# Kernel tuning notes

Measured on AMD Instinct MI355X. Metric: run time of the kernel, lower is better.

Reference implementation:

```python
import jax, jax.numpy as jnp
import numpy as np

EPS = 1e-12


def pairwise_sqdist(x, y):
    # x: (B, N, 3), y: (B, M, 3) -> (B, N, M) squared euclidean distances
    xx = jnp.sum(x * x, axis=-1)              # (B, N)
    yy = jnp.sum(y * y, axis=-1)              # (B, M)
    xy = jnp.einsum('bnd,bmd->bnm', x, y)     # (B, N, M)
    d = xx[:, :, None] + yy[None_ if False else yy[:, None, :].shape and 0 or ...] if False else xx[:, :, None] + yy[:, None, :] - 2.0 * xy
    return jnp.maximum(d, 0.0)


def chamfer_l1(x, y):
    # pytorch3d/PoinTr-style ChamferDistanceL1:
    # mean over points of sqrt(min squared dist), averaged over both directions
    d = pairwise_sqdist(x, y)                 # (B, N, M)
    d1 = jnp.min(d, axis=2)                   # (B, N) x -> nearest y
    d2 = jnp.min(d, axis=1)                   # (B, M) y -> nearest x
    d1 = jnp.sqrt(jnp.maximum(d1, EPS))
    d2 = jnp.sqrt(jnp.maximum(d2, EPS))
    return 0.5 * (jnp.mean(d1) + jnp.mean(d2))


def knn1_gather(x, y):
    # For each point in x (B,N,3), find nearest neighbor in y (B,M,3) (K=1)
    # and gather it -> (B, N, 3). Matches knn_points + knn_gather + squeeze.
    d = pairwise_sqdist(x, y)                 # (B, N, M)
    idx = jnp.argmin(d, axis=2)               # (B, N) int
    return jnp.take_along_axis(y, idx[:, :, None], axis=1)  # (B, N, 3)


def volume_with_wedge(p):
    # wedge-product volume over consecutive point triples:
    # V = sum_i (p_i x p_{i+1}) . p_{i+2} / 6  -> (B,)
    c = jnp.cross(p[:, :-2, :], p[:, 1:-1, :])  # (B, N-2, 3)
    return jnp.sum(jnp.einsum('bnd,bnd->bn', c, p[:, 2:, :]), axis=-1) / 6.0


def setup_inputs() -> dict:
    key = jax.random.key(0)
    k1, k2, k3 = jax.random.split(key, 3)
    B, Nc, Nf, M = 2, 512, 8192, 8192
    return {
        'source_coarse': jax.random.normal(k1, (B, Nc, 3), dtype=jnp.float32),
        'source_fine': jax.random.normal(k2, (B, Nf, 3), dtype=jnp.float32),
        'target_points': jax.random.normal(k3, (B, M, 3), dtype=jnp.float32),
    }


def reference(source_coarse, source_fine, target_points):
    lambda_rot = lambda_ref = lambda_align = lambda_geo = 1.0
    B = source_fine.shape[0]
    axis = jnp.broadcast_to(jnp.array([0.0, 0.0, 1.0], dtype=source_fine.dtype), (B, 3))
    plane_normal = jnp.broadcast_to(jnp.array([0.0, 1.0, 0.0], dtype=source_fine.dtype), (B, 3))

    # KNN (K=1) gather of nearest target point for each fine source point
    new_target = knn1_gather(source_fine, target_points)  # (B, Nf, 3)

    # alignment (Chamfer L1) losses
    loss_align_coarse = chamfer_l1(source_coarse, target_points)
    loss_align_fine = chamfer_l1(source_fine, target_points)

    # rotational symmetry loss
    in_proj = jnp.einsum('bij,bj->bi', source_fine, axis)      # (B, Nf)
    re_proj = jnp.einsum('bij,bj->bi', new_target, axis)
    loss_rot = jnp.mean((jnp.linalg.norm(in_proj, axis=-1) - jnp.linalg.norm(re_proj, axis=-1)) ** 2)

    # reflectional symmetry loss
    pn = plane_normal / jnp.linalg.norm(plane_normal, axis=-1, keepdims=True)
    in_dist = jnp.einsum('bij,bj->bi', source_fine, pn)
    re_dist = jnp.einsum('bij,bj->bi', new_target, pn)
    loss_ref = jnp.mean((in_dist - re_dist) ** 2)

    # geometric consistency (wedge-product volume) loss
    loss_geo = jnp.mean((volume_with_wedge(source_fine) - volume_with_wedge(new_target)) ** 2)

    total = (lambda_rot * loss_rot + lambda_ref * loss_ref
             + lambda_align * loss_align_coarse + lambda_align * loss_align_fine
             + lambda_geo * loss_geo)
    return total
```

## Files before the change

### kernel.cpp

```cpp
#include <hip/hip_runtime.h>
#include <stdint.h>
#include <float.h>

using u64 = unsigned long long;
typedef float v2f __attribute__((ext_vector_type(2)));

constexpr int B_ = 2;
constexpr int NC = 512;
constexpr int NF = 8192;
constexpr int MT = 8192;

constexpr int TPB = 256;
constexpr int CFF = 32;
constexpr int CCR = 128;
constexpr int CCC = 8;
constexpr int TAIL_BLOCKS = 196;

#define DEVINL __device__ __forceinline__

template<bool ARGMIN, int R2t, int NJ>
DEVINL void pairmin_phase(const float* __restrict__ P, const float* __restrict__ Q,
                          int nP, int nQ, int b, int row_base, int j0,
                          int chunk, int nRowsTot,
                          u64* __restrict__ outPack, unsigned* __restrict__ outVal)
{
#pragma clang fp contract(off)
    const int tid = threadIdx.x;

    v2f tx0[R2t], tx1[R2t], tx2[R2t], txx[R2t], dbest[R2t];
    int jb[2 * R2t];
    #pragma unroll
    for (int r = 0; r < R2t; ++r) {
        const int row0 = row_base + tid + (2 * r) * TPB;
        const int row1 = row_base + tid + (2 * r + 1) * TPB;
        const float* p0 = P + ((size_t)b * nP + row0) * 3;
        const float* p1 = P + ((size_t)b * nP + row1) * 3;
        float a0 = p0[0], a1 = p0[1], a2 = p0[2];
        float e0 = p1[0], e1 = p1[1], e2 = p1[2];
        tx0[r] = v2f{2.0f * a0, 2.0f * e0};
        tx1[r] = v2f{2.0f * a1, 2.0f * e1};
        tx2[r] = v2f{2.0f * a2, 2.0f * e2};
        txx[r] = v2f{(a0*a0 + a1*a1) + a2*a2, (e0*e0 + e1*e1) + e2*e2};
        dbest[r] = v2f{FLT_MAX, FLT_MAX};
        jb[2 * r] = 0; jb[2 * r + 1] = 0;
    }

    const float* qbase = Q + (size_t)b * nQ * 3;

    float q0r[8], q1r[8], q2r[8];
    #pragma unroll
    for (int u = 0; u < 8; ++u) {
        const float* qp = qbase + (size_t)(j0 + u) * 3;
        q0r[u] = qp[0]; q1r[u] = qp[1]; q2r[u] = qp[2];
    }

    for (int jj = 0; jj < NJ; jj += 8) {
        #pragma unroll
        for (int u = 0; u < 8; ++u) {
            const float q0 = q0r[u], q1 = q1r[u], q2 = q2r[u];
            int pj = jj + 8 + u;  pj = (pj < NJ) ? pj : (NJ - 1);
            const float* qp = qbase + (size_t)(j0 + pj) * 3;
            q0r[u] = qp[0]; q1r[u] = qp[1]; q2r[u] = qp[2];

            const float qq = (q0*q0 + q1*q1) + q2*q2;
            const int j = j0 + jj + u;
            #pragma unroll
            for (int r = 0; r < R2t; ++r) {
                v2f s = (tx0[r] * q0 + tx1[r] * q1) + tx2[r] * q2;
                v2f d = (txx[r] + qq) - s;
                if (ARGMIN) {
                    bool c0 = d.x < dbest[r].x;
                    bool c1 = d.y < dbest[r].y;
                    dbest[r].x = c0 ? d.x : dbest[r].x;
                    dbest[r].y = c1 ? d.y : dbest[r].y;
                    jb[2 * r]     = c0 ? j : jb[2 * r];
                    jb[2 * r + 1] = c1 ? j : jb[2 * r + 1];
                } else {
                    dbest[r] = __builtin_elementwise_min(dbest[r], d);
                }
            }
        }
    }

    const v2f vzero = {0.0f, 0.0f};
    const size_t o0 = (size_t)chunk * nRowsTot + (size_t)b * nP;
    #pragma unroll
    for (int r = 0; r < R2t; ++r) {
        v2f dcl = __builtin_elementwise_max(dbest[r], vzero);
        const int row0 = row_base + tid + (2 * r) * TPB;
        const int row1 = row_base + tid + (2 * r + 1) * TPB;
        if (ARGMIN) {
            outPack[o0 + row0] = ((u64)__float_as_uint(dcl.x) << 32) | (unsigned)jb[2 * r];
            outPack[o0 + row1] = ((u64)__float_as_uint(dcl.y) << 32) | (unsigned)jb[2 * r + 1];
        } else {
            outVal[o0 + row0] = __float_as_uint(dcl.x);
            outVal[o0 + row1] = __float_as_uint(dcl.y);
        }
    }
}

__global__ __launch_bounds__(TPB, 4) void pairmin_all(
    const float* __restrict__ coarse, const float* __restrict__ fine,
    const float* __restrict__ tgt,
    u64* __restrict__ pfr, unsigned* __restrict__ pfc,
    unsigned* __restrict__ pcr, unsigned* __restrict__ pcc,
    unsigned* __restrict__ counter)
{
    const int bx = blockIdx.x;
    if (bx == 0 && threadIdx.x == 0) *counter = 0;
    const int b   = bx >> 8;
    const int sub = bx & 255;
    const int g   = sub >> 5;
    const int c   = sub & 31;

    pairmin_phase<true, 2, 256>(fine, tgt, NF, MT, b, g * 1024, c * 256,
                                c, B_ * NF, pfr, nullptr);
    pairmin_phase<false, 2, 256>(tgt, fine, MT, NF, b, g * 1024, c * 256,
                                 c, B_ * MT, nullptr, pfc);
    if (sub < 128) {
        pairmin_phase<false, 1, 64>(coarse, tgt, NC, MT, b, 0, sub * 64,
                                    sub, B_ * NC, nullptr, pcr);
    } else {
        const int s2 = sub - 128;
        const int rg = s2 & 15;
        const int jc = s2 >> 4;
        pairmin_phase<false, 1, 64>(tgt, coarse, MT, NC, b, rg * 512, jc * 64,
                                    jc, B_ * MT, nullptr, pcc);
    }
}

__global__ __launch_bounds__(TPB) void tail_all(
    const float* __restrict__ fine, const float* __restrict__ tgt,
    const u64* __restrict__ pfr, const unsigned* __restrict__ pfc,
    const unsigned* __restrict__ pcr, const unsigned* __restrict__ pcc,
    double* __restrict__ bs, unsigned* __restrict__ counter,
    float* __restrict__ out)
{
    __shared__ float sp[TPB + 2][3], yp[TPB + 2][3];
    __shared__ double redw[4][9];
    __shared__ double lred[4][13];
    __shared__ int lastflag;
    const int bx = blockIdx.x, tid = threadIdx.x;
    const int wave = tid >> 6, lane = tid & 63;

    double v_s = 0, v_d2f = 0, v_d1c = 0, v_d2c = 0, v_yd2 = 0, v_zs = 0, v_zt = 0;
    double vs = 0, vt = 0;
    int role_b = 0;

    if (bx < 64) {
        const int base = bx * TPB;
        const int g = base + tid;
        const int b = base >> 13;  role_b = b;
        u64 best = pfr[g];
        #pragma unroll
        for (int cc = 1; cc < CFF; ++cc) {
            u64 p = pfr[(size_t)cc * (B_ * NF) + g];
            best = p < best ? p : best;
        }
        float d1 = __uint_as_float((unsigned)(best >> 32));
        int idx  = (int)(best & 0xffffffffULL);
        float s = sqrtf(fmaxf(d1, 1e-12f));
        const float* y  = tgt  + ((size_t)b * MT + idx) * 3;
        const float* sr = fine + (size_t)g * 3;
        float y0 = y[0],  y1 = y[1],  y2 = y[2];
        float s0 = sr[0], s1 = sr[1], s2 = sr[2];
        yp[tid][0] = y0; yp[tid][1] = y1; yp[tid][2] = y2;
        sp[tid][0] = s0; sp[tid][1] = s1; sp[tid][2] = s2;
        const int base_b = base & (NF - 1);
        if (tid < 2 && base_b + TPB + tid < NF) {
            int g2 = base + TPB + tid;
            u64 b2 = pfr[g2];
            #pragma unroll
            for (int cc = 1; cc < CFF; ++cc) {
                u64 p = pfr[(size_t)cc * (B_ * NF) + g2];
                b2 = p < b2 ? p : b2;
            }
            int i2 = (int)(b2 & 0xffffffffULL);
            const float* yh = tgt  + ((size_t)b * MT + i2) * 3;
            const float* sh = fine + (size_t)g2 * 3;
            #pragma unroll
            for (int k = 0; k < 3; ++k) { yp[TPB + tid][k] = yh[k]; sp[TPB + tid][k] = sh[k]; }
        }
        __syncthreads();
        v_s = s;
        float yd = s1 - y1;
        v_yd2 = (double)(yd * yd);
        v_zs  = (double)(s2 * s2);
        v_zt  = (double)(y2 * y2);
        int rb = base_b + tid;
        if (rb <= NF - 3) {
            {
                const float* a = sp[tid]; const float* c2 = sp[tid+1]; const float* e = sp[tid+2];
                float c0 = a[1]*c2[2] - a[2]*c2[1];
                float c1 = a[2]*c2[0] - a[0]*c2[2];
                float c2v = a[0]*c2[1] - a[1]*c2[0];
                vs = (double)(c0*e[0] + c1*e[1] + c2v*e[2]);
            }
            {
                const float* a = yp[tid]; const float* c2 = yp[tid+1]; const float* e = yp[tid+2];
                float c0 = a[1]*c2[2] - a[2]*c2[1];
                float c1 = a[2]*c2[0] - a[0]*c2[2];
                float c2v = a[0]*c2[1] - a[1]*c2[0];
                vt = (double)(c0*e[0] + c1*e[1] + c2v*e[2]);
            }
        }
    } else if (bx < 128) {
        const int g = (bx - 64) * TPB + tid;
        unsigned best = pfc[g];
        #pragma unroll
        for (int cc = 1; cc < CFF; ++cc) best = min(best, pfc[(size_t)cc * (B_ * MT) + g]);
        v_d2f = (double)sqrtf(fmaxf(__uint_as_float(best), 1e-12f));
    } else if (bx < 132) {
        const int g = (bx - 128) * TPB + tid;
        unsigned best = pcr[g];
        #pragma unroll 16
        for (int cc = 1; cc < CCR; ++cc) best = min(best, pcr[(size_t)cc * (B_ * NC) + g]);
        v_d1c = (double)sqrtf(fmaxf(__uint_as_float(best), 1e-12f));
    } else {
        const int g = (bx - 132) * TPB + tid;
        unsigned best = pcc[g];
        #pragma unroll
        for (int cc = 1; cc < CCC; ++cc) best = min(best, pcc[(size_t)cc * (B_ * MT) + g]);
        v_d2c = (double)sqrtf(fmaxf(__uint_as_float(best), 1e-12f));
    }

    double r9[9] = {v_s, v_d2f, v_d1c, v_d2c, v_yd2, v_zs, v_zt, vs, vt};
    for (int o = 32; o; o >>= 1) {
        #pragma unroll
        for (int k = 0; k < 9; ++k) r9[k] += __shfl_down(r9[k], o);
    }
    if (lane == 0) {
        #pragma unroll
        for (int k = 0; k < 9; ++k) redw[wave][k] = r9[k];
    }
    __syncthreads();
    if (tid == 0) {
        double t9[9];
        #pragma unroll
        for (int k = 0; k < 9; ++k)
            t9[k] = redw[0][k] + redw[1][k] + redw[2][k] + redw[3][k];
        double* o = bs + (size_t)bx * 16;
        #pragma unroll
        for (int k = 0; k < 16; ++k) o[k] = 0.0;
        o[0] = t9[0]; o[1] = t9[1]; o[2] = t9[2]; o[3] = t9[3]; o[4] = t9[4];
        o[5 + role_b]  = t9[5];
        o[7 + role_b]  = t9[6];
        o[9 + role_b]  = t9[7];
        o[11 + role_b] = t9[8];
        __threadfence();
        unsigned old = atomicAdd(counter, 1u);
        lastflag = (old == TAIL_BLOCKS - 1);
    }
    __syncthreads();
    if (!lastflag) return;

    __threadfence();
    double c13[13];
    if (tid < TAIL_BLOCKS) {
        const double* p = bs + (size_t)tid * 16;
        #pragma unroll
        for (int k = 0; k < 13; ++k) c13[k] = p[k];
    } else {
        #pragma unroll
        for (int k = 0; k < 13; ++k) c13[k] = 0.0;
    }
    for (int o = 32; o; o >>= 1) {
        #pragma unroll
        for (int k = 0; k < 13; ++k) c13[k] += __shfl_down(c13[k], o);
    }
    if (lane == 0) {
        #pragma unroll
        for (int k = 0; k < 13; ++k) lred[wave][k] = c13[k];
    }
    __syncthreads();
    if (tid == 0) {
        double S[13];
        #pragma unroll
        for (int k = 0; k < 13; ++k)
            S[k] = lred[0][k] + lred[1][k] + lred[2][k] + lred[3][k];
        double m_d1f = S[0] / (double)(B_ * NF);
        double m_d2f = S[1] / (double)(B_ * MT);
        double m_d1c = S[2] / (double)(B_ * NC);
        double m_d2c = S[3] / (double)(B_ * MT);
        double loss_align_fine   = 0.5 * (m_d1f + m_d2f);
        double loss_align_coarse = 0.5 * (m_d1c + m_d2c);
        double loss_ref = S[4] / (double)(B_ * NF);
        double loss_rot = 0.0, loss_geo = 0.0;
        for (int b = 0; b < B_; ++b) {
            double dn = sqrt(S[5 + b]) - sqrt(S[7 + b]);
            loss_rot += dn * dn;
            double dv = (S[9 + b] - S[11 + b]) / 6.0;
            loss_geo += dv * dv;
        }
        loss_rot /= (double)B_;
        loss_geo /= (double)B_;
        out[0] = (float)(loss_rot + loss_ref + loss_align_coarse + loss_align_fine + loss_geo);
    }
}

extern "C" void kernel_launch(void* const* d_in, const int* in_sizes, int n_in,
                              void* d_out, int out_size, void* d_ws, size_t ws_size,
                              hipStream_t stream)
{
    const float* src_coarse = (const float*)d_in[0];
    const float* src_fine   = (const float*)d_in[1];
    const float* tgt        = (const float*)d_in[2];
    float* out = (float*)d_out;
    char*  ws  = (char*)d_ws;

    u64*      pfr     = (u64*)(ws);
    unsigned* pfc     = (unsigned*)(ws + 4194304);
    unsigned* pcr     = (unsigned*)(ws + 6291456);
    unsigned* pcc     = (unsigned*)(ws + 6815744);
    double*   bs      = (double*)(ws + 7340032);
    unsigned* counter = (unsigned*)(ws + 7365120);

    pairmin_all<<<dim3(512), TPB, 0, stream>>>(
        src_coarse, src_fine, tgt, pfr, pfc, pcr, pcc, counter);
    tail_all<<<dim3(TAIL_BLOCKS), TPB, 0, stream>>>(
        src_fine, tgt, pfr, pfc, pcr, pcc, bs, counter, out);
}
```

Before: 141.2 us.

## Stage query points in LDS and split fine passes across blocks with more rows

Each block now loads its chunk of query points, together with their precomputed squared norms, into a shared-memory float4 tile. The inner loop reads that tile with double-buffered register loads instead of streaming strided global loads and recomputing the norm for every row. Blocks are split so the fine→target argmin and the target→fine min run in separate blocks, and each thread handles 8 rows instead of 4. Launch bounds drop to 2 waves per SIMD, which allows more registers but lowers occupancy, and the added __syncthreads barriers cost some time.

```diff
diff --git a/kernel.cpp b/kernel.cpp
--- a/kernel.cpp
+++ b/kernel.cpp
@@ -22,7 +22,8 @@
 DEVINL void pairmin_phase(const float* __restrict__ P, const float* __restrict__ Q,
                           int nP, int nQ, int b, int row_base, int j0,
                           int chunk, int nRowsTot,
-                          u64* __restrict__ outPack, unsigned* __restrict__ outVal)
+                          u64* __restrict__ outPack, unsigned* __restrict__ outVal,
+                          float4* tile)
 {
 #pragma clang fp contract(off)
     const int tid = threadIdx.x;
@@ -45,41 +46,45 @@
         jb[2 * r] = 0; jb[2 * r + 1] = 0;
     }
 
-    const float* qbase = Q + (size_t)b * nQ * 3;
-
-    float q0r[8], q1r[8], q2r[8];
+    __syncthreads();
+    if (tid < NJ) {
+        const float* q = Q + ((size_t)b * nQ + j0 + tid) * 3;
+        float q0 = q[0], q1 = q[1], q2 = q[2];
+        tile[tid] = make_float4(q0, q1, q2, (q0*q0 + q1*q1) + q2*q2);
+    }
+    __syncthreads();
+
+    auto PROC = [&](const float4 qv, const int j) {
+#pragma clang fp contract(off)
+        #pragma unroll
+        for (int r = 0; r < R2t; ++r) {
+            v2f s = (tx0[r] * qv.x + tx1[r] * qv.y) + tx2[r] * qv.z;
+            v2f d = (txx[r] + qv.w) - s;
+            if (ARGMIN) {
+                bool c0 = d.x < dbest[r].x;
+                bool c1 = d.y < dbest[r].y;
+                dbest[r].x = c0 ? d.x : dbest[r].x;
+                dbest[r].y = c1 ? d.y : dbest[r].y;
+                jb[2 * r]     = c0 ? j : jb[2 * r];
+                jb[2 * r + 1] = c1 ? j : jb[2 * r + 1];
+            } else {
+                dbest[r] = __builtin_elementwise_min(dbest[r], d);
+            }
+        }
+    };
+
+    float4 qa[4], qb[4];
     #pragma unroll
-    for (int u = 0; u < 8; ++u) {
-        const float* qp = qbase + (size_t)(j0 + u) * 3;
-        q0r[u] = qp[0]; q1r[u] = qp[1]; q2r[u] = qp[2];
-    }
-
+    for (int u = 0; u < 4; ++u) qa[u] = tile[u];
     for (int jj = 0; jj < NJ; jj += 8) {
         #pragma unroll
-        for (int u = 0; u < 8; ++u) {
-            const float q0 = q0r[u], q1 = q1r[u], q2 = q2r[u];
-            int pj = jj + 8 + u;  pj = (pj < NJ) ? pj : (NJ - 1);
-            const float* qp = qbase + (size_t)(j0 + pj) * 3;
-            q0r[u] = qp[0]; q1r[u] = qp[1]; q2r[u] = qp[2];
-
-            const float qq = (q0*q0 + q1*q1) + q2*q2;
-            const int j = j0 + jj + u;
-            #pragma unroll
-            for (int r = 0; r < R2t; ++r) {
-                v2f s = (tx0[r] * q0 + tx1[r] * q1) + tx2[r] * q2;
-                v2f d = (txx[r] + qq) - s;
-                if (ARGMIN) {
-                    bool c0 = d.x < dbest[r].x;
-                    bool c1 = d.y < dbest[r].y;
-                    dbest[r].x = c0 ? d.x : dbest[r].x;
-                    dbest[r].y = c1 ? d.y : dbest[r].y;
-                    jb[2 * r]     = c0 ? j : jb[2 * r];
-                    jb[2 * r + 1] = c1 ? j : jb[2 * r + 1];
-                } else {
-                    dbest[r] = __builtin_elementwise_min(dbest[r], d);
-                }
-            }
-        }
+        for (int u = 0; u < 4; ++u) qb[u] = tile[jj + 4 + u];
+        #pragma unroll
+        for (int u = 0; u < 4; ++u) PROC(qa[u], j0 + jj + u);
+        #pragma unroll
+        for (int u = 0; u < 4; ++u) qa[u] = tile[(jj + 8 + u) & (NJ - 1)];
+        #pragma unroll
+        for (int u = 0; u < 4; ++u) PROC(qb[u], j0 + jj + 4 + u);
     }
 
     const v2f vzero = {0.0f, 0.0f};
@@ -99,33 +104,29 @@
     }
 }
 
-__global__ __launch_bounds__(TPB, 4) void pairmin_all(
+__global__ __launch_bounds__(TPB, 2) void pairmin_all(
     const float* __restrict__ coarse, const float* __restrict__ fine,
     const float* __restrict__ tgt,
     u64* __restrict__ pfr, unsigned* __restrict__ pfc,
     unsigned* __restrict__ pcr, unsigned* __restrict__ pcc,
     unsigned* __restrict__ counter)
 {
+    __shared__ float4 tile[256];
     const int bx = blockIdx.x;
     if (bx == 0 && threadIdx.x == 0) *counter = 0;
-    const int b   = bx >> 8;
-    const int sub = bx & 255;
-    const int g   = sub >> 5;
-    const int c   = sub & 31;
-
-    pairmin_phase<true, 2, 256>(fine, tgt, NF, MT, b, g * 1024, c * 256,
-                                c, B_ * NF, pfr, nullptr);
-    pairmin_phase<false, 2, 256>(tgt, fine, MT, NF, b, g * 1024, c * 256,
-                                 c, B_ * MT, nullptr, pfc);
-    if (sub < 128) {
-        pairmin_phase<false, 1, 64>(coarse, tgt, NC, MT, b, 0, sub * 64,
-                                    sub, B_ * NC, nullptr, pcr);
+    if (bx < 256) {
+        const int b = bx >> 7, g = (bx >> 5) & 3, c = bx & 31;
+        pairmin_phase<true, 4, 256>(fine, tgt, NF, MT, b, g * 2048, c * 256,
+                                    c, B_ * NF, pfr, nullptr, tile);
+        pairmin_phase<false, 1, 64>(coarse, tgt, NC, MT, bx >> 7, 0, (bx & 127) * 64,
+                                    bx & 127, B_ * NC, nullptr, pcr, tile);
     } else {
-        const int s2 = sub - 128;
-        const int rg = s2 & 15;
-        const int jc = s2 >> 4;
-        pairmin_phase<false, 1, 64>(tgt, coarse, MT, NC, b, rg * 512, jc * 64,
-                                    jc, B_ * MT, nullptr, pcc);
+        const int i = bx - 256;
+        const int b = i >> 7, g = (i >> 5) & 3, c = i & 31;
+        pairmin_phase<false, 4, 256>(tgt, fine, MT, NF, b, g * 2048, c * 256,
+                                     c, B_ * MT, nullptr, pfc, tile);
+        pairmin_phase<false, 1, 64>(tgt, coarse, MT, NC, i >> 7, ((i >> 3) & 15) * 512,
+                                    (i & 7) * 64, i & 7, B_ * MT, nullptr, pcc, tile);
     }
 }
 
```

Measured after the change: 120.3 us. 14.7% less time.
